# Optimization experiments

Hardware: AMD Instinct MI355X
Metric: run time of the kernel (lower is better)

## Reference

```python
import jax, jax.numpy as jnp
import numpy as np
from jax import lax

B, T, D, H, C = 64, 512, 1024, 2048, 5


def _linear_params(key, fan_in, fan_out):
    # mimic torch.nn.Linear default init: U(-1/sqrt(fan_in), 1/sqrt(fan_in))
    kw, kb = jax.random.split(key)
    bound = 1.0 / np.sqrt(fan_in)
    w = jax.random.uniform(kw, (fan_out, fan_in), jnp.float32, -bound, bound)
    b = jax.random.uniform(kb, (fan_out,), jnp.float32, -bound, bound)
    return w, b


def setup_inputs() -> dict:
    key = jax.random.key(0)
    ks = jax.random.split(key, 5)
    inputs = jax.random.normal(ks[0], (B, T, D), jnp.float32)
    W_w, W_b = _linear_params(ks[1], D, H)
    U_w, U_b = _linear_params(ks[2], H, H)
    V1_w, V1_b = _linear_params(ks[3], H, H)
    V2_w, V2_b = _linear_params(ks[4], H, C)
    return {"inputs": inputs, "W_w": W_w, "W_b": W_b, "U_w": U_w, "U_b": U_b,
            "V1_w": V1_w, "V1_b": V1_b, "V2_w": V2_w, "V2_b": V2_b}


def reference(inputs, W_w, W_b, U_w, U_b, V1_w, V1_b, V2_w, V2_b):
    # Precompute input projection for all timesteps: [B, T, H]
    xw = jnp.einsum('btd,hd->bth', inputs, W_w) + W_b

    def step(h, xt):  # h: [B,H], xt: [B,H]
        h_new = jax.nn.relu(xt + h @ U_w.T + U_b)
        return h_new, None

    h0 = jnp.zeros((inputs.shape[0], U_w.shape[0]), inputs.dtype)
    h_last, _ = lax.scan(step, h0, jnp.swapaxes(xw, 0, 1))  # scan over time

    z1 = jax.nn.relu(h_last @ V1_w.T + V1_b)      # [B, H]
    z2 = jax.nn.relu(z1 @ V2_w.T + V2_b)          # [B, 5]
    return jax.nn.log_softmax(z2, axis=-1)
```

## Files before the change

kernel.cpp:

```cpp
#include <hip/hip_runtime.h>
#include <math.h>

typedef __bf16 bf16_t;
typedef __bf16 bf16x4 __attribute__((ext_vector_type(4)));
typedef __bf16 bf16x8 __attribute__((ext_vector_type(8)));
typedef float f32x4 __attribute__((ext_vector_type(4)));
typedef unsigned long long u64;

#define MFMA_16x16x32(A, B, C) __builtin_amdgcn_mfma_f32_16x16x32_bf16((A), (B), (C), 0, 0, 0)

static constexpr int Bn = 64;
static constexpr int Tn = 512;
static constexpr int Dn = 1024;
static constexpr int Hn = 2048;
static constexpr int Cn = 5;
static constexpr int NGB = 64;
static constexpr int NGRP = 4;
static constexpr int NBT = NGB * NGRP;
static constexpr int NW = 16;

#define SWZ64(row, kb)  ((((row) * 64) + (kb)) ^ (((row) & 3) << 4))

__global__ __launch_bounds__(256) void cvt_bf16_k(const float* __restrict__ in,
                                                  bf16_t* __restrict__ out, int n4) {
  int i = blockIdx.x * 256 + threadIdx.x;
  if (i >= n4) return;
  float4 v = reinterpret_cast<const float4*>(in)[i];
  bf16x4 o;
  o[0] = (bf16_t)v.x; o[1] = (bf16_t)v.y; o[2] = (bf16_t)v.z; o[3] = (bf16_t)v.w;
  reinterpret_cast<bf16x4*>(out)[i] = o;
}

__global__ __launch_bounds__(256) void cvt_hilo_k(const float* __restrict__ in,
                                                  bf16_t* __restrict__ hi,
                                                  bf16_t* __restrict__ lo, int n4) {
  int i = blockIdx.x * 256 + threadIdx.x;
  if (i >= n4) return;
  float4 v = reinterpret_cast<const float4*>(in)[i];
  float f[4] = {v.x, v.y, v.z, v.w};
  bf16x4 h, l;
#pragma unroll
  for (int j = 0; j < 4; ++j) {
    bf16_t hb = (bf16_t)f[j];
    h[j] = hb;
    l[j] = (bf16_t)(f[j] - (float)hb);
  }
  reinterpret_cast<bf16x4*>(hi)[i] = h;
  reinterpret_cast<bf16x4*>(lo)[i] = l;
}

__global__ __launch_bounds__(256) void gemm_xw_k(const float* __restrict__ A,
                                                 const bf16_t* __restrict__ Bw,
                                                 const float* __restrict__ bias,
                                                 bf16_t* __restrict__ C) {
  constexpr int K = Dn;
  constexpr int N = Hn;
  constexpr int NT = K / 32;
  __shared__ char As[2][128 * 64];
  __shared__ char Bs[2][128 * 64];

  const int tid = threadIdx.x;
  const int lane = tid & 63;
  const int wv = tid >> 6;
  const int wm = (wv >> 1) * 64;
  const int wn = (wv & 1) * 64;
  const int cl = lane & 15;
  const int kh = lane >> 4;
  const long m0 = (long)blockIdx.y * 128;
  const long n0 = (long)blockIdx.x * 128;

  const int srow = tid >> 1;
  const int scolb = (tid & 1) * 32;

  f32x4 acc[4][4] = {};
  float4 pa[4];
  uint4 pb[2];

  auto issue = [&](int kt) {
    const float* ap = A + (m0 + srow) * K + kt * 32 + (tid & 1) * 16;
#pragma unroll
    for (int i = 0; i < 4; ++i) pa[i] = reinterpret_cast<const float4*>(ap)[i];
    const bf16_t* bp = Bw + (n0 + srow) * K + kt * 32 + (tid & 1) * 16;
    pb[0] = reinterpret_cast<const uint4*>(bp)[0];
    pb[1] = reinterpret_cast<const uint4*>(bp)[1];
  };
  auto commit = [&](int buf) {
    bf16x8 a0, a1;
    a0[0] = (bf16_t)pa[0].x; a0[1] = (bf16_t)pa[0].y; a0[2] = (bf16_t)pa[0].z; a0[3] = (bf16_t)pa[0].w;
    a0[4] = (bf16_t)pa[1].x; a0[5] = (bf16_t)pa[1].y; a0[6] = (bf16_t)pa[1].z; a0[7] = (bf16_t)pa[1].w;
    a1[0] = (bf16_t)pa[2].x; a1[1] = (bf16_t)pa[2].y; a1[2] = (bf16_t)pa[2].z; a1[3] = (bf16_t)pa[2].w;
    a1[4] = (bf16_t)pa[3].x; a1[5] = (bf16_t)pa[3].y; a1[6] = (bf16_t)pa[3].z; a1[7] = (bf16_t)pa[3].w;
    *reinterpret_cast<bf16x8*>(&As[buf][SWZ64(srow, scolb)]) = a0;
    *reinterpret_cast<bf16x8*>(&As[buf][SWZ64(srow, scolb + 16)]) = a1;
    *reinterpret_cast<uint4*>(&Bs[buf][SWZ64(srow, scolb)]) = pb[0];
    *reinterpret_cast<uint4*>(&Bs[buf][SWZ64(srow, scolb + 16)]) = pb[1];
  };

  issue(0);
  commit(0);
  for (int kt = 0; kt < NT; ++kt) {
    const int buf = kt & 1;
    __syncthreads();
    if (kt + 1 < NT) issue(kt + 1);
    bf16x8 af[4], bfr[4];
#pragma unroll
    for (int i = 0; i < 4; ++i)
      af[i] = *reinterpret_cast<const bf16x8*>(&As[buf][SWZ64(wm + i * 16 + cl, kh * 16)]);
#pragma unroll
    for (int j = 0; j < 4; ++j)
      bfr[j] = *reinterpret_cast<const bf16x8*>(&Bs[buf][SWZ64(wn + j * 16 + cl, kh * 16)]);
#pragma unroll
    for (int i = 0; i < 4; ++i)
#pragma unroll
      for (int j = 0; j < 4; ++j)
        acc[i][j] = MFMA_16x16x32(af[i], bfr[j], acc[i][j]);
    if (kt + 1 < NT) commit((kt + 1) & 1);
  }

  const int rl4 = kh * 4;
#pragma unroll
  for (int j = 0; j < 4; ++j) {
    const long gcol = n0 + wn + j * 16 + cl;
    const float bv = bias[gcol];
#pragma unroll
    for (int i = 0; i < 4; ++i) {
      const long grow = m0 + wm + i * 16 + rl4;
#pragma unroll
      for (int q = 0; q < 4; ++q)
        C[(grow + q) * N + gcol] = (bf16_t)(acc[i][j][q] + bv);
    }
  }
}

__global__ __launch_bounds__(1024, 1) void scan_k(
    const bf16_t* __restrict__ Uhi, const bf16_t* __restrict__ Ulo,
    const float* __restrict__ Ub, const bf16_t* __restrict__ XW,
    bf16_t* __restrict__ Hc, long Hstep, int rot,
    const bf16_t* __restrict__ V1w, const float* __restrict__ V1b,
    float* __restrict__ Z1,
    const float* __restrict__ V2w, const float* __restrict__ V2b,
    float* __restrict__ out, unsigned* __restrict__ slots) {
  extern __shared__ char smem[];
  float* redb = (float*)smem;

  const int tid = threadIdx.x;
  const int lane = tid & 63;
  const int wv = tid >> 6;
  const int cl = lane & 15;
  const int kh = lane >> 4;
  const int bid = blockIdx.x;
  const int g = (bid & 7) >> 1;
  const int j = (bid >> 3) * 2 + (bid & 1);
  const int n0 = j * 32;
  const int row0 = g * 16;
  unsigned* gflags = slots + (size_t)g * (NGB * 2 * 32);

  bf16x8 Ubh[2][4], Ubl[2][4];
#pragma unroll
  for (int ct = 0; ct < 2; ++ct)
#pragma unroll
    for (int ksub = 0; ksub < 4; ++ksub) {
      const long uoff = (long)(n0 + ct * 16 + cl) * Hn + wv * 128 + ksub * 32 + kh * 8;
      Ubh[ct][ksub] = *reinterpret_cast<const bf16x8*>(Uhi + uoff);
      Ubl[ct][ksub] = *reinterpret_cast<const bf16x8*>(Ulo + uoff);
    }

  const bool storer = (wv < 2);
  const int srow = (wv & 1) * 8 + (lane >> 3);
  const int scol = (lane & 7) * 4;
  float4 bv4 = {0.f, 0.f, 0.f, 0.f};
  if (storer) bv4 = *reinterpret_cast<const float4*>(Ub + n0 + scol);
  const long xw_off = (long)(row0 + srow) * (Tn * Hn) + n0 + scol;

  bf16x4 ad = {};
  if (storer) ad = *reinterpret_cast<const bf16x4*>(XW + xw_off);

  bf16_t* hin = Hc;
  bf16_t* hout = Hc + Hstep;

  for (int t = 0; t < Tn; ++t) {
    const bf16_t* arow = hin + (long)(row0 + cl) * Hn + wv * 128 + kh * 8;

    bf16x8 a[4];
#pragma unroll
    for (int ksub = 0; ksub < 4; ++ksub)
      a[ksub] = *reinterpret_cast<const bf16x8*>(arow + ksub * 32);

    f32x4 acch[2] = {}, accl[2] = {};
#pragma unroll
    for (int ksub = 0; ksub < 4; ++ksub) {
      acch[0] = MFMA_16x16x32(a[ksub], Ubh[0][ksub], acch[0]);
      accl[0] = MFMA_16x16x32(a[ksub], Ubl[0][ksub], accl[0]);
      acch[1] = MFMA_16x16x32(a[ksub], Ubh[1][ksub], acch[1]);
      accl[1] = MFMA_16x16x32(a[ksub], Ubl[1][ksub], accl[1]);
    }

    float* red = redb + (t & 1) * 8192;
#pragma unroll
    for (int ct = 0; ct < 2; ++ct)
#pragma unroll
      for (int q = 0; q < 4; ++q)
        red[wv * 512 + (kh * 4 + q) * 32 + ct * 16 + cl] = acch[ct][q] + accl[ct][q];

    __syncthreads();

    if (storer) {
      const int ri = srow * 32 + scol;
      float4 s = {0.f, 0.f, 0.f, 0.f};
#pragma unroll
      for (int w = 0; w < NW; ++w) {
        float4 p = *reinterpret_cast<const float4*>(&red[w * 512 + ri]);
        s.x += p.x; s.y += p.y; s.z += p.z; s.w += p.w;
      }
      bf16x4 hv;
      hv[0] = (bf16_t)fmaxf(s.x + bv4.x + (float)ad[0], 0.f);
      hv[1] = (bf16_t)fmaxf(s.y + bv4.y + (float)ad[1], 0.f);
      hv[2] = (bf16_t)fmaxf(s.z + bv4.z + (float)ad[2], 0.f);
      hv[3] = (bf16_t)fmaxf(s.w + bv4.w + (float)ad[3], 0.f);
      __hip_atomic_store(
          reinterpret_cast<u64*>(hout + (long)(row0 + srow) * Hn + n0 + scol),
          *reinterpret_cast<const u64*>(&hv), __ATOMIC_RELAXED,
          __HIP_MEMORY_SCOPE_AGENT);
      asm volatile("s_waitcnt vmcnt(0)" ::: "memory");
      if (lane == 0)
        __hip_atomic_store(gflags + (size_t)(j * 2 + wv) * 32, (unsigned)(t + 1),
                           __ATOMIC_RELAXED, __HIP_MEMORY_SCOPE_AGENT);
      if (t + 1 < Tn)
        ad = *reinterpret_cast<const bf16x4*>(XW + xw_off + (long)(t + 1) * Hn);
    }

    const unsigned tgt = (unsigned)(t + 1);
    if (wv == 0) {
      for (;;) {
        unsigned a0 = __hip_atomic_load(gflags + (size_t)lane * 32,
                                        __ATOMIC_RELAXED, __HIP_MEMORY_SCOPE_AGENT);
        unsigned b0 = __hip_atomic_load(gflags + (size_t)(lane + 64) * 32,
                                        __ATOMIC_RELAXED, __HIP_MEMORY_SCOPE_AGENT);
        if (__all((a0 >= tgt) && (b0 >= tgt))) break;
      }
      if (!rot) __builtin_amdgcn_fence(__ATOMIC_ACQUIRE, "agent");
    }
    asm volatile("" ::: "memory");
    __syncthreads();

    bf16_t* nn = hout;
    hout = rot ? (hout + Hstep) : hin;
    hin = nn;
  }

  {
    const bf16_t* arow = hin + (long)(row0 + cl) * Hn + wv * 128 + kh * 8;
    f32x4 z[2] = {};
#pragma unroll
    for (int ksub = 0; ksub < 4; ++ksub) {
      bf16x8 a0 = *reinterpret_cast<const bf16x8*>(arow + ksub * 32);
#pragma unroll
      for (int ct = 0; ct < 2; ++ct) {
        const long voff = (long)(n0 + ct * 16 + cl) * Hn + wv * 128 + ksub * 32 + kh * 8;
        bf16x8 b0 = *reinterpret_cast<const bf16x8*>(V1w + voff);
        z[ct] = MFMA_16x16x32(a0, b0, z[ct]);
      }
    }
    float* red = redb;
#pragma unroll
    for (int ct = 0; ct < 2; ++ct)
#pragma unroll
      for (int q = 0; q < 4; ++q)
        red[wv * 512 + (kh * 4 + q) * 32 + ct * 16 + cl] = z[ct][q];
    __syncthreads();
    if (storer) {
      const int ri = srow * 32 + scol;
      float4 s = {0.f, 0.f, 0.f, 0.f};
#pragma unroll
      for (int w = 0; w < NW; ++w) {
        float4 p = *reinterpret_cast<const float4*>(&red[w * 512 + ri]);
        s.x += p.x; s.y += p.y; s.z += p.z; s.w += p.w;
      }
      float4 vb = *reinterpret_cast<const float4*>(V1b + n0 + scol);
      float4 o;
      o.x = fmaxf(s.x + vb.x, 0.f);
      o.y = fmaxf(s.y + vb.y, 0.f);
      o.z = fmaxf(s.z + vb.z, 0.f);
      o.w = fmaxf(s.w + vb.w, 0.f);
      *reinterpret_cast<float4*>(Z1 + (long)(row0 + srow) * Hn + n0 + scol) = o;
    }
  }

  {
    unsigned* fbar = slots + (size_t)NGRP * NGB * 2 * 32;
    __syncthreads();
    if (tid == 0)
      __hip_atomic_store(fbar + (size_t)bid * 32, 1u,
                         __ATOMIC_RELEASE, __HIP_MEMORY_SCOPE_AGENT);
    if (tid < 64) {
      for (;;) {
        unsigned a = __hip_atomic_load(fbar + (size_t)tid * 32,
                                       __ATOMIC_RELAXED, __HIP_MEMORY_SCOPE_AGENT);
        unsigned b = __hip_atomic_load(fbar + (size_t)(tid + 64) * 32,
                                       __ATOMIC_RELAXED, __HIP_MEMORY_SCOPE_AGENT);
        unsigned c = __hip_atomic_load(fbar + (size_t)(tid + 128) * 32,
                                       __ATOMIC_RELAXED, __HIP_MEMORY_SCOPE_AGENT);
        unsigned d = __hip_atomic_load(fbar + (size_t)(tid + 192) * 32,
                                       __ATOMIC_RELAXED, __HIP_MEMORY_SCOPE_AGENT);
        if (__all((int)((a >= 1u) && (b >= 1u) && (c >= 1u) && (d >= 1u)))) break;
      }
      __builtin_amdgcn_fence(__ATOMIC_ACQUIRE, "agent");
    }
    __syncthreads();
  }

  if (bid < Bn) {
    const int b = bid;
    float p[Cn] = {0.f, 0.f, 0.f, 0.f, 0.f};
    for (int jj = tid; jj < Hn; jj += 1024) {
      const float x = Z1[(long)b * Hn + jj];
#pragma unroll
      for (int c = 0; c < Cn; ++c) p[c] += x * V2w[(long)c * Hn + jj];
    }
#pragma unroll
    for (int c = 0; c < Cn; ++c)
      for (int off = 32; off; off >>= 1) p[c] += __shfl_down(p[c], off, 64);

    float* redh = reinterpret_cast<float*>(smem);
    if (lane == 0) {
#pragma unroll
      for (int c = 0; c < Cn; ++c) redh[c * NW + wv] = p[c];
    }
    __syncthreads();
    if (tid == 0) {
      float z[Cn];
      float mx = 0.f;
#pragma unroll
      for (int c = 0; c < Cn; ++c) {
        float s16 = 0.f;
#pragma unroll
        for (int w = 0; w < NW; ++w) s16 += redh[c * NW + w];
        z[c] = fmaxf(s16 + V2b[c], 0.f);
        mx = fmaxf(mx, z[c]);
      }
      float s = 0.f;
#pragma unroll
      for (int c = 0; c < Cn; ++c) s += expf(z[c] - mx);
      const float ls = logf(s);
#pragma unroll
      for (int c = 0; c < Cn; ++c) out[b * Cn + c] = z[c] - mx - ls;
    }
  }
}

extern "C" void kernel_launch(void* const* d_in, const int* in_sizes, int n_in,
                              void* d_out, int out_size, void* d_ws, size_t ws_size,
                              hipStream_t stream) {
  const float* inputs = (const float*)d_in[0];
  const float* W_w = (const float*)d_in[1];
  const float* W_b = (const float*)d_in[2];
  const float* U_w = (const float*)d_in[3];
  const float* U_b = (const float*)d_in[4];
  const float* V1_w = (const float*)d_in[5];
  const float* V1_b = (const float*)d_in[6];
  const float* V2_w = (const float*)d_in[7];
  const float* V2_b = (const float*)d_in[8];
  float* out = (float*)d_out;

  size_t off = 0;
  auto alloc = [&](size_t bytes) {
    void* p = (char*)d_ws + off;
    off += (bytes + 255) & ~(size_t)255;
    return p;
  };
  bf16_t* Wbf = (bf16_t*)alloc((size_t)Hn * Dn * 2);
  bf16_t* Uhi = (bf16_t*)alloc((size_t)Hn * Hn * 2);
  bf16_t* Ulo = (bf16_t*)alloc((size_t)Hn * Hn * 2);
  bf16_t* V1bf = (bf16_t*)alloc((size_t)Hn * Hn * 2);
  bf16_t* XW = (bf16_t*)alloc((size_t)Bn * Tn * Hn * 2);
  float* Z1 = (float*)alloc((size_t)Bn * Hn * 4);
  const size_t slots_bytes = (size_t)(NGRP * NGB * 2 * 32 + NBT * 32) * 4;
  unsigned* slots = (unsigned*)alloc(slots_bytes);

  const size_t slot_bytes = (size_t)Bn * Hn * 2;
  const size_t rot_bytes = (size_t)(Tn + 1) * slot_bytes;
  const int rot = (ws_size - off) >= (rot_bytes + 256) ? 1 : 0;
  bf16_t* Hc = (bf16_t*)alloc(rot ? rot_bytes : 2 * slot_bytes);
  (void)ws_size;

  (void)hipFuncSetAttribute((const void*)scan_k,
                            hipFuncAttributeMaxDynamicSharedMemorySize, 65536);

  cvt_bf16_k<<<(Hn * Dn / 4 + 255) / 256, 256, 0, stream>>>(W_w, Wbf, Hn * Dn / 4);
  cvt_hilo_k<<<(Hn * Hn / 4 + 255) / 256, 256, 0, stream>>>(U_w, Uhi, Ulo, Hn * Hn / 4);
  cvt_bf16_k<<<(Hn * Hn / 4 + 255) / 256, 256, 0, stream>>>(V1_w, V1bf, Hn * Hn / 4);

  gemm_xw_k<<<dim3(Hn / 128, (Bn * Tn) / 128), 256, 0, stream>>>(inputs, Wbf, W_b, XW);

  (void)hipMemsetAsync(Hc, 0, slot_bytes, stream);
  (void)hipMemsetAsync(slots, 0, slots_bytes, stream);

  scan_k<<<NBT, 1024, 65536, stream>>>(Uhi, Ulo, U_b, XW, Hc, (long)Bn * Hn, rot,
                                       V1bf, V1_b, Z1, V2_w, V2_b, out, slots);
}
```

Measured before the change: 2.600 ms.

## Replace per-step flag barrier with per-wave mailbox signaling in recurrent scan

New measurement: 3.429 ms. 31.9% more time.

```diff
diff --git a/kernel.cpp b/kernel.cpp
--- a/kernel.cpp
+++ b/kernel.cpp
@@ -153,7 +153,8 @@
   const int j = (bid >> 3) * 2 + (bid & 1);
   const int n0 = j * 32;
   const int row0 = g * 16;
-  unsigned* gflags = slots + (size_t)g * (NGB * 2 * 32);
+  unsigned* mb = slots + (size_t)g * (NGB * NW * 8);
+  const int moff_cons = (j * NW + wv) * 8 + (lane & 7);
 
   bf16x8 Ubh[2][4], Ubl[2][4];
 #pragma unroll
@@ -168,6 +169,8 @@
   const bool storer = (wv < 2);
   const int srow = (wv & 1) * 8 + (lane >> 3);
   const int scol = (lane & 7) * 4;
+  const int moff_prod = (lane * NW + (j >> 2)) * 8 + (j & 3) * 2 + wv;
+
   float4 bv4 = {0.f, 0.f, 0.f, 0.f};
   if (storer) bv4 = *reinterpret_cast<const float4*>(Ub + n0 + scol);
   const long xw_off = (long)(row0 + srow) * (Tn * Hn) + n0 + scol;
@@ -179,6 +182,17 @@
   bf16_t* hout = Hc + Hstep;
 
   for (int t = 0; t < Tn; ++t) {
+    {
+      const unsigned tgt = (unsigned)t;
+      for (;;) {
+        unsigned v = __hip_atomic_load(mb + moff_cons, __ATOMIC_RELAXED,
+                                       __HIP_MEMORY_SCOPE_AGENT);
+        if (__all((int)(v >= tgt))) break;
+      }
+      asm volatile("" ::: "memory");
+      if (!rot) __builtin_amdgcn_fence(__ATOMIC_ACQUIRE, "agent");
+    }
+
     const bf16_t* arow = hin + (long)(row0 + cl) * Hn + wv * 128 + kh * 8;
 
     bf16x8 a[4];
@@ -222,26 +236,11 @@
           *reinterpret_cast<const u64*>(&hv), __ATOMIC_RELAXED,
           __HIP_MEMORY_SCOPE_AGENT);
       asm volatile("s_waitcnt vmcnt(0)" ::: "memory");
-      if (lane == 0)
-        __hip_atomic_store(gflags + (size_t)(j * 2 + wv) * 32, (unsigned)(t + 1),
-                           __ATOMIC_RELAXED, __HIP_MEMORY_SCOPE_AGENT);
+      __hip_atomic_store(mb + moff_prod, (unsigned)(t + 1), __ATOMIC_RELAXED,
+                         __HIP_MEMORY_SCOPE_AGENT);
       if (t + 1 < Tn)
         ad = *reinterpret_cast<const bf16x4*>(XW + xw_off + (long)(t + 1) * Hn);
     }
-
-    const unsigned tgt = (unsigned)(t + 1);
-    if (wv == 0) {
-      for (;;) {
-        unsigned a0 = __hip_atomic_load(gflags + (size_t)lane * 32,
-                                        __ATOMIC_RELAXED, __HIP_MEMORY_SCOPE_AGENT);
-        unsigned b0 = __hip_atomic_load(gflags + (size_t)(lane + 64) * 32,
-                                        __ATOMIC_RELAXED, __HIP_MEMORY_SCOPE_AGENT);
-        if (__all((a0 >= tgt) && (b0 >= tgt))) break;
-      }
-      if (!rot) __builtin_amdgcn_fence(__ATOMIC_ACQUIRE, "agent");
-    }
-    asm volatile("" ::: "memory");
-    __syncthreads();
 
     bf16_t* nn = hout;
     hout = rot ? (hout + Hstep) : hin;
@@ -249,6 +248,15 @@
   }
 
   {
+    const unsigned tgt = (unsigned)Tn;
+    for (;;) {
+      unsigned v = __hip_atomic_load(mb + moff_cons, __ATOMIC_RELAXED,
+                                     __HIP_MEMORY_SCOPE_AGENT);
+      if (__all((int)(v >= tgt))) break;
+    }
+    asm volatile("" ::: "memory");
+    if (!rot) __builtin_amdgcn_fence(__ATOMIC_ACQUIRE, "agent");
+
     const bf16_t* arow = hin + (long)(row0 + cl) * Hn + wv * 128 + kh * 8;
     f32x4 z[2] = {};
 #pragma unroll
@@ -287,7 +295,7 @@
   }
 
   {
-    unsigned* fbar = slots + (size_t)NGRP * NGB * 2 * 32;
+    unsigned* fbar = slots + (size_t)NGRP * NGB * NW * 8;
     __syncthreads();
     if (tid == 0)
       __hip_atomic_store(fbar + (size_t)bid * 32, 1u,
@@ -374,7 +382,7 @@
   bf16_t* V1bf = (bf16_t*)alloc((size_t)Hn * Hn * 2);
   bf16_t* XW = (bf16_t*)alloc((size_t)Bn * Tn * Hn * 2);
   float* Z1 = (float*)alloc((size_t)Bn * Hn * 4);
-  const size_t slots_bytes = (size_t)(NGRP * NGB * 2 * 32 + NBT * 32) * 4;
+  const size_t slots_bytes = (size_t)(NGRP * NGB * NW * 8 + NBT * 32) * 4;
   unsigned* slots = (unsigned*)alloc(slots_bytes);
 
   const size_t slot_bytes = (size_t)Bn * Hn * 2;
```
